# Kernel tuning notes

Hardware: AMD Instinct MI355X
Metric: run time of the kernel (lower is better)

The kernel has to match this reference:

```python
import jax, jax.numpy as jnp
import numpy as np
from jax import lax

B, T, J = 32, 256, 24

def _build_adj(n):
    parent = [-1,0,0,0,1,2,3,4,5,6,7,8,9,9,9,12,13,14,16,17,18,19,20,21]
    a = np.eye(n, dtype=np.float32)
    for c in range(min(n, len(parent))):
        p = parent[c]
        if 0 <= p < n:
            a[c, p] = 1.0
            a[p, c] = 1.0
    if n > len(parent):
        for j in range(len(parent), n - 1):
            a[j, j + 1] = 1.0
            a[j + 1, j] = 1.0
    d = np.clip(a.sum(1, keepdims=True), 1.0, None)
    return jnp.asarray(a / d)

ADJ = _build_adj(J)  # [J, J] degree-normalized SMPL adjacency


def _axis_angle_to_rot6d(aa):
    # aa: [..., 3] -> [..., 6] (first two columns of rotation matrix, row-major)
    angle = jnp.linalg.norm(aa, axis=-1)
    axis = aa / (angle[..., None] + 1e-8)
    x, y, z = axis[..., 0], axis[..., 1], axis[..., 2]
    zeros = jnp.zeros_like(x)
    K = jnp.stack([zeros, -z, y, z, zeros, -x, -y, x, zeros], axis=-1)
    K = K.reshape(axis.shape[:-1] + (3, 3))
    eye = jnp.eye(3, dtype=aa.dtype)
    cos = jnp.cos(angle)[..., None, None]
    sin = jnp.sin(angle)[..., None, None]
    outer = axis[..., :, None] * axis[..., None, :]
    rot = cos * eye + (1.0 - cos) * outer + sin * K
    return rot[..., :2].reshape(aa.shape[:-1] + (6,))


def _bn(x, p, eps=1e-5):
    # inference BatchNorm2d; p = stacked [gamma, beta, mean, var], each [C]
    g, b, m, v = p
    s = g / jnp.sqrt(v + eps)
    return x * s[None, :, None, None] + (b - m * s)[None, :, None, None]


def _block(x, gcn_w, gcn_b, bn1, tcn_w, tcn_b, bn2, res_w=None, res_b=None):
    # 1x1 conv (pointwise channel mix)
    y = jnp.einsum('oc,bctj->botj', gcn_w, x) + gcn_b[None, :, None, None]
    # graph aggregation over joints
    y = jnp.einsum('bctj,jk->bctk', y, ADJ)
    y = jax.nn.relu(_bn(y, bn1))
    # temporal conv (3,1), padding (1,0); dropout is identity at inference
    y = lax.conv_general_dilated(y, tcn_w, (1, 1), ((1, 1), (0, 0)),
                                 dimension_numbers=('NCHW', 'OIHW', 'NCHW'))
    y = _bn(y + tcn_b[None, :, None, None], bn2)
    if res_w is None:
        r = x
    else:
        r = jnp.einsum('oc,bctj->botj', res_w, x) + res_b[None, :, None, None]
    return jax.nn.relu(y + r)


def setup_inputs() -> dict:
    key = jax.random.key(0)
    ks = iter(jax.random.split(key, 64))
    def rn(shape, s=0.05):
        return jax.random.normal(next(ks), shape, jnp.float32) * s
    def bnp(c):
        g = jax.random.uniform(next(ks), (c,), jnp.float32) * 0.5 + 0.75
        b = rn((c,), 0.1)
        m = rn((c,), 0.1)
        v = jax.random.uniform(next(ks), (c,), jnp.float32) * 0.5 + 0.5
        return jnp.stack([g, b, m, v])
    return {
        'x': jax.random.normal(next(ks), (B, T, J, 3), jnp.float32),
        'b1_gcn_w': rn((128, 6)), 'b1_gcn_b': rn((128,)), 'b1_bn1': bnp(128),
        'b1_tcn_w': rn((128, 128, 3, 1)), 'b1_tcn_b': rn((128,)), 'b1_bn2': bnp(128),
        'b1_res_w': rn((128, 6)), 'b1_res_b': rn((128,)),
        'b2_gcn_w': rn((128, 128)), 'b2_gcn_b': rn((128,)), 'b2_bn1': bnp(128),
        'b2_tcn_w': rn((128, 128, 3, 1)), 'b2_tcn_b': rn((128,)), 'b2_bn2': bnp(128),
        'b3_gcn_w': rn((256, 128)), 'b3_gcn_b': rn((256,)), 'b3_bn1': bnp(256),
        'b3_tcn_w': rn((256, 256, 3, 1)), 'b3_tcn_b': rn((256,)), 'b3_bn2': bnp(256),
        'b3_res_w': rn((256, 128)), 'b3_res_b': rn((256,)),
        'out_w': rn((512, 256)), 'out_b': rn((512,)),
    }


def reference(x, b1_gcn_w, b1_gcn_b, b1_bn1, b1_tcn_w, b1_tcn_b, b1_bn2, b1_res_w, b1_res_b,
              b2_gcn_w, b2_gcn_b, b2_bn1, b2_tcn_w, b2_tcn_b, b2_bn2,
              b3_gcn_w, b3_gcn_b, b3_bn1, b3_tcn_w, b3_tcn_b, b3_bn2, b3_res_w, b3_res_b,
              out_w, out_b):
    rot6d = _axis_angle_to_rot6d(x)                 # [B,T,J,6]
    f = jnp.transpose(rot6d, (0, 3, 1, 2))          # [B,6,T,J]
    f = _block(f, b1_gcn_w, b1_gcn_b, b1_bn1, b1_tcn_w, b1_tcn_b, b1_bn2, b1_res_w, b1_res_b)
    f = _block(f, b2_gcn_w, b2_gcn_b, b2_bn1, b2_tcn_w, b2_tcn_b, b2_bn2)
    f = _block(f, b3_gcn_w, b3_gcn_b, b3_bn1, b3_tcn_w, b3_tcn_b, b3_bn2, b3_res_w, b3_res_b)
    pooled = f.mean(axis=(2, 3))                    # [B,256]
    mu = pooled @ out_w.T + out_b                   # [B,512]
    return mu
```

## Files before the change

### kernel.cpp

```cpp
#include <hip/hip_runtime.h>
#include <math.h>

#define J_ 24
#define T_ 256
#define B_ 32

typedef short short8v __attribute__((ext_vector_type(8)));
typedef float f32x4  __attribute__((ext_vector_type(4)));

__device__ __forceinline__ short f2bf(float f) {
    unsigned u = __float_as_uint(f);
    u += 0x7fffu + ((u >> 16) & 1u);
    return (short)(u >> 16);
}
__device__ __forceinline__ float bf2f(short s) {
    return __uint_as_float(((unsigned)(unsigned short)s) << 16);
}

__device__ __constant__ int d_parent[24] = {-1,0,0,0,1,2,3,4,5,6,7,8,9,9,9,12,13,14,16,17,18,19,20,21};

__global__ void adj_init_kernel(float* __restrict__ adj_out) {
    __shared__ float s_adj[576];
    const int tid = threadIdx.x;
    for (int i = tid; i < 576; i += 256) {
        const int j = i / 24, k = i % 24;
        float a = (j == k || d_parent[k] == j || d_parent[j] == k) ? 1.f : 0.f;
        float d = 0.f;
        for (int kk = 0; kk < 24; ++kk)
            d += (j == kk || d_parent[kk] == j || d_parent[j] == kk) ? 1.f : 0.f;
        const float v = a / fmaxf(d, 1.f);
        s_adj[i] = v;
        adj_out[i] = v;
    }
    __syncthreads();
    if (tid < 24) {
        float cs = 0.f;
        for (int j = 0; j < 24; ++j) cs += s_adj[j*24 + tid];
        adj_out[576 + tid] = cs;
        int n = 0;
        for (int j = 0; j < 24; ++j) {
            const float w = s_adj[j*24 + tid];
            if (w != 0.f && n < 8) {
                adj_out[600 + tid*8 + n] = w;
                adj_out[792 + tid*8 + n] = (float)j;
                ++n;
            }
        }
        for (; n < 8; ++n) { adj_out[600 + tid*8 + n] = 0.f; adj_out[792 + tid*8 + n] = 0.f; }
    }
}

__global__ __launch_bounds__(256) void prep_kernel(
    const float* __restrict__ w1t, const float* __restrict__ bn1_2,
    const float* __restrict__ w2t, const float* __restrict__ bn2_2,
    const float* __restrict__ w3t, const float* __restrict__ bn3_2,
    const float* __restrict__ g2w, const float* __restrict__ bn2_1,
    const float* __restrict__ g3w, const float* __restrict__ bn3_1,
    const float* __restrict__ r3w,
    short* __restrict__ wt1b, short* __restrict__ wt2b, short* __restrict__ wt3b,
    short* __restrict__ gw2b, short* __restrict__ gw3b, short* __restrict__ rw3b)
{
    const int i = blockIdx.x * 256 + threadIdx.x;
    if (i < 49152) {
        const int o = i / 384, r = i % 384, dt = r / 128, c = r % 128;
        const float s = bn1_2[o] * rsqrtf(bn1_2[384 + o] + 1e-5f);
        wt1b[i] = f2bf(s * w1t[(o*128 + c)*3 + dt]);
    } else if (i < 98304) {
        const int j = i - 49152;
        const int o = j / 384, r = j % 384, dt = r / 128, c = r % 128;
        const float s = bn2_2[o] * rsqrtf(bn2_2[384 + o] + 1e-5f);
        wt2b[j] = f2bf(s * w2t[(o*128 + c)*3 + dt]);
    } else if (i < 294912) {
        const int j = i - 98304;
        const int o = j / 768, r = j % 768, dt = r / 256, c = r % 256;
        const float s = bn3_2[o] * rsqrtf(bn3_2[768 + o] + 1e-5f);
        wt3b[j] = f2bf(s * w3t[(o*256 + c)*3 + dt]);
    } else if (i < 311296) {
        const int j = i - 294912;
        const int o = j / 128;
        const float s = bn2_1[o] * rsqrtf(bn2_1[384 + o] + 1e-5f);
        gw2b[j] = f2bf(s * g2w[j]);
    } else if (i < 344064) {
        const int j = i - 311296;
        const int o = j / 128;
        const float s = bn3_1[o] * rsqrtf(bn3_1[768 + o] + 1e-5f);
        gw3b[j] = f2bf(s * g3w[j]);
    } else if (i < 376832) {
        const int j = i - 344064;
        rw3b[j] = f2bf(r3w[j]);
    }
}

#define LDS_SZ   52320
#define FA_OFF   26112
#define X6_OFF   40320
#define XA6_OFF  44928
#define TBL_OFF  50688

__global__ __launch_bounds__(512) void block1_kernel(
    const float* __restrict__ x,
    const float* __restrict__ gw1, const float* __restrict__ gb1, const float* __restrict__ bn1,
    const float* __restrict__ rw1, const float* __restrict__ rb1,
    const float* __restrict__ bn12, const float* __restrict__ tb1, const short* __restrict__ wt1b,
    const short* __restrict__ gw2b, const float* __restrict__ gb2, const float* __restrict__ bn21,
    const float* __restrict__ adjp,
    short* __restrict__ f1_out, short* __restrict__ h2_out)
{
    __shared__ char smem[LDS_SZ];
    float* s_x6  = (float*)(smem + X6_OFF);
    float* s_xa6 = (float*)(smem + XA6_OFF);
    float* s_cw  = (float*)(smem + TBL_OFF);
    int*   s_ci  = (int*)  (smem + TBL_OFF + 768);
    float* s_cs  = (float*)(smem + TBL_OFF + 1536);

    const int r0 = blockIdx.x * 96;
    const int bstart = (r0 / 6144) * 6144;
    const int bend = bstart + 6144;
    const int tid = threadIdx.x;
    const int l = tid & 63, wid = tid >> 6;
    const int m0w = (wid >> 2) * 48;
    const int n0w = (wid & 3) * 32;
    const int lr = l & 15, lk = l >> 4;

    if (tid < 192) { s_cw[tid] = adjp[600 + tid]; s_ci[tid] = (int)adjp[792 + tid]; }
    else if (tid < 216) s_cs[tid - 192] = adjp[576 + (tid - 192)];
    if (tid < 144) {
        const int gr = r0 - 24 + tid;
        float o0=0,o1=0,o2=0,o3=0,o4=0,o5=0;
        if (gr >= bstart && gr < bend) {
            const float ax = x[gr*3+0], ay = x[gr*3+1], az = x[gr*3+2];
            const float angle = sqrtf(ax*ax + ay*ay + az*az);
            const float inv = 1.f / (angle + 1e-8f);
            const float ux = ax*inv, uy = ay*inv, uz = az*inv;
            const float c = cosf(angle), s = sinf(angle), omc = 1.f - c;
            o0 = c + omc*ux*ux;   o1 = omc*ux*uy - s*uz;
            o2 = omc*uy*ux + s*uz; o3 = c + omc*uy*uy;
            o4 = omc*uz*ux - s*uy; o5 = omc*uz*uy + s*ux;
        }
        float* p = s_x6 + tid*8;
        p[0]=o0; p[1]=o1; p[2]=o2; p[3]=o3; p[4]=o4; p[5]=o5;
    }
    __syncthreads();
    for (int idx = tid; idx < 864; idx += 512) {
        const int hr = idx / 6, c = idx % 6;
        const int k = hr % 24, sl = (hr / 24) * 24;
        float a = 0.f;
        #pragma unroll
        for (int u = 0; u < 8; ++u)
            a = fmaf(s_cw[k*8+u], s_x6[(sl + s_ci[k*8+u])*8 + c], a);
        s_xa6[hr*8 + c] = a;
    }
    __syncthreads();
    {
        const int og = (tid & 15) * 8;
        const int rg0 = tid >> 4;
        float wgf[48], s1v[8], t1v[8], g1v[8];
        {
            const float4* gwp = (const float4*)(gw1 + og*6);
            #pragma unroll
            for (int i = 0; i < 12; ++i) ((float4*)wgf)[i] = gwp[i];
            #pragma unroll
            for (int e = 0; e < 8; ++e) {
                const int o = og + e;
                const float s1 = bn1[o] * rsqrtf(bn1[384 + o] + 1e-5f);
                s1v[e] = s1;
                t1v[e] = bn1[128 + o] - bn1[256 + o] * s1;
                g1v[e] = s1 * gb1[o];
            }
        }
        for (int hr = rg0; hr < 144; hr += 32) {
            const int gr = r0 - 24 + hr;
            short8v hv = {0,0,0,0,0,0,0,0};
            if (gr >= bstart && gr < bend) {
                const float4 v4 = *(const float4*)(s_xa6 + hr*8);
                const float2 v2 = *(const float2*)(s_xa6 + hr*8 + 4);
                const float cs = s_cs[hr % 24];
                #pragma unroll
                for (int e = 0; e < 8; ++e) {
                    float a = v4.x * wgf[e*6+0];
                    a = fmaf(v4.y, wgf[e*6+1], a);
                    a = fmaf(v4.z, wgf[e*6+2], a);
                    a = fmaf(v4.w, wgf[e*6+3], a);
                    a = fmaf(v2.x, wgf[e*6+4], a);
                    a = fmaf(v2.y, wgf[e*6+5], a);
                    hv[e] = f2bf(fmaxf(s1v[e]*a + t1v[e] + g1v[e]*cs, 0.f));
                }
            }
            *(short8v*)(smem + hr*256 + ((og*2) ^ ((hr&7)<<4))) = hv;
        }
    }
    __syncthreads();
    f32x4 acc[3][2];
    #pragma unroll
    for (int mi = 0; mi < 3; ++mi)
        #pragma unroll
        for (int ni = 0; ni < 2; ++ni) acc[mi][ni] = (f32x4){0.f,0.f,0.f,0.f};
    #pragma unroll
    for (int dt = 0; dt < 3; ++dt) {
        #pragma unroll
        for (int kc = 0; kc < 4; ++kc) {
            short8v bfr[2], afr[3];
            #pragma unroll
            for (int ni = 0; ni < 2; ++ni) {
                const int n = n0w + ni*16 + lr;
                bfr[ni] = *(const short8v*)(wt1b + (size_t)n*384 + dt*128 + kc*32 + lk*8);
            }
            #pragma unroll
            for (int mi = 0; mi < 3; ++mi) {
                const int row = m0w + dt*24 + mi*16 + lr;
                afr[mi] = *(const short8v*)(smem + row*256 + ((kc*64 + lk*16) ^ ((row&7)<<4)));
            }
            #pragma unroll
            for (int mi = 0; mi < 3; ++mi)
                #pragma unroll
                for (int ni = 0; ni < 2; ++ni)
                    acc[mi][ni] = __builtin_amdgcn_mfma_f32_16x16x32_bf16(afr[mi], bfr[ni], acc[mi][ni], 0, 0, 0);
        }
    }
    __syncthreads();
    #pragma unroll
    for (int ni = 0; ni < 2; ++ni) {
        const int o = n0w + ni*16 + lr;
        const float s2 = bn12[o] * rsqrtf(bn12[384 + o] + 1e-5f);
        const float bias = (bn12[128 + o] - bn12[256 + o]*s2) + s2*tb1[o];
        float wr[6];
        #pragma unroll
        for (int c = 0; c < 6; ++c) wr[c] = rw1[o*6 + c];
        const float rb = rb1[o];
        #pragma unroll
        for (int mi = 0; mi < 3; ++mi)
            #pragma unroll
            for (int rg = 0; rg < 4; ++rg) {
                const int rl = m0w + mi*16 + lk*4 + rg;
                const float4 v4 = *(const float4*)(s_x6 + (rl+24)*8);
                const float2 v2 = *(const float2*)(s_x6 + (rl+24)*8 + 4);
                float r = fmaf(v4.x, wr[0], rb);
                r = fmaf(v4.y, wr[1], r);
                r = fmaf(v4.z, wr[2], r);
                r = fmaf(v4.w, wr[3], r);
                r = fmaf(v2.x, wr[4], r);
                r = fmaf(v2.y, wr[5], r);
                const short hv = f2bf(fmaxf(acc[mi][ni][rg] + bias + r, 0.f));
                f1_out[(size_t)(r0 + rl)*128 + o] = hv;
                *(short*)(smem + rl*272 + o*2) = hv;
            }
    }
    __syncthreads();
    for (int task = tid; task < 96*16; task += 512) {
        const int row = task >> 4, cg = task & 15;
        const int k = row % 24, sl = (row / 24) * 24;
        float a[8] = {0,0,0,0,0,0,0,0};
        #pragma unroll
        for (int u = 0; u < 8; ++u) {
            const float wgt = s_cw[k*8+u];
            const short8v v = *(const short8v*)(smem + (sl + s_ci[k*8+u])*272 + cg*16);
            #pragma unroll
            for (int e = 0; e < 8; ++e) a[e] = fmaf(wgt, bf2f(v[e]), a[e]);
        }
        short8v o8;
        #pragma unroll
        for (int e = 0; e < 8; ++e) o8[e] = f2bf(a[e]);
        *(short8v*)(smem + FA_OFF + row*256 + ((cg*16) ^ ((row&7)<<4))) = o8;
    }
    __syncthreads();
    #pragma unroll
    for (int mi = 0; mi < 3; ++mi)
        #pragma unroll
        for (int ni = 0; ni < 2; ++ni) acc[mi][ni] = (f32x4){0.f,0.f,0.f,0.f};
    #pragma unroll
    for (int kc = 0; kc < 4; ++kc) {
        short8v bfr[2], afr[3];
        #pragma unroll
        for (int ni = 0; ni < 2; ++ni) {
            const int n = n0w + ni*16 + lr;
            bfr[ni] = *(const short8v*)(gw2b + (size_t)n*128 + kc*32 + lk*8);
        }
        #pragma unroll
        for (int mi = 0; mi < 3; ++mi) {
            const int row = m0w + mi*16 + lr;
            afr[mi] = *(const short8v*)(smem + FA_OFF + row*256 + ((kc*64 + lk*16) ^ ((row&7)<<4)));
        }
        #pragma unroll
        for (int mi = 0; mi < 3; ++mi)
            #pragma unroll
            for (int ni = 0; ni < 2; ++ni)
                acc[mi][ni] = __builtin_amdgcn_mfma_f32_16x16x32_bf16(afr[mi], bfr[ni], acc[mi][ni], 0, 0, 0);
    }
    #pragma unroll
    for (int ni = 0; ni < 2; ++ni) {
        const int o = n0w + ni*16 + lr;
        const float s = bn21[o] * rsqrtf(bn21[384 + o] + 1e-5f);
        const float t = bn21[128 + o] - bn21[256 + o]*s;
        const float g = s * gb2[o];
        #pragma unroll
        for (int mi = 0; mi < 3; ++mi)
            #pragma unroll
            for (int rg = 0; rg < 4; ++rg) {
                const int rl = m0w + mi*16 + lk*4 + rg;
                h2_out[(size_t)(r0 + rl)*128 + o] = f2bf(fmaxf(acc[mi][ni][rg] + t + g*s_cs[rl % 24], 0.f));
            }
    }
}

__global__ __launch_bounds__(512) void block2_kernel(
    const short* __restrict__ h2, const short* __restrict__ wt2b,
    const float* __restrict__ bn22, const float* __restrict__ tb2,
    const short* __restrict__ f1,
    const short* __restrict__ gw3b, const float* __restrict__ gb3, const float* __restrict__ bn31,
    const float* __restrict__ adjp,
    short* __restrict__ f2_out, short* __restrict__ h3_out)
{
    __shared__ char smem[LDS_SZ];
    float* s_cw  = (float*)(smem + TBL_OFF);
    int*   s_ci  = (int*)  (smem + TBL_OFF + 768);
    float* s_cs  = (float*)(smem + TBL_OFF + 1536);

    const int r0 = blockIdx.x * 96;
    const int bstart = (r0 / 6144) * 6144;
    const int bend = bstart + 6144;
    const int tid = threadIdx.x;
    const int l = tid & 63, wid = tid >> 6;
    const int m0w = (wid >> 2) * 48;
    const int lr = l & 15, lk = l >> 4;

    if (tid < 192) { s_cw[tid] = adjp[600 + tid]; s_ci[tid] = (int)adjp[792 + tid]; }
    else if (tid < 216) s_cs[tid - 192] = adjp[576 + (tid - 192)];
    for (int ch = tid; ch < 144*16; ch += 512) {
        const int row = ch >> 4, cg = ch & 15;
        const int gr = r0 - 24 + row;
        float4 v = make_float4(0.f,0.f,0.f,0.f);
        if (gr >= bstart && gr < bend)
            v = *(const float4*)(h2 + (size_t)gr*128 + cg*8);
        *(float4*)(smem + row*256 + ((cg*16) ^ ((row&7)<<4))) = v;
    }
    __syncthreads();
    {
        const int n0w = (wid & 3) * 32;
        f32x4 acc[3][2];
        #pragma unroll
        for (int mi = 0; mi < 3; ++mi)
            #pragma unroll
            for (int ni = 0; ni < 2; ++ni) acc[mi][ni] = (f32x4){0.f,0.f,0.f,0.f};
        #pragma unroll
        for (int dt = 0; dt < 3; ++dt) {
            #pragma unroll
            for (int kc = 0; kc < 4; ++kc) {
                short8v bfr[2], afr[3];
                #pragma unroll
                for (int ni = 0; ni < 2; ++ni) {
                    const int n = n0w + ni*16 + lr;
                    bfr[ni] = *(const short8v*)(wt2b + (size_t)n*384 + dt*128 + kc*32 + lk*8);
                }
                #pragma unroll
                for (int mi = 0; mi < 3; ++mi) {
                    const int row = m0w + dt*24 + mi*16 + lr;
                    afr[mi] = *(const short8v*)(smem + row*256 + ((kc*64 + lk*16) ^ ((row&7)<<4)));
                }
                #pragma unroll
                for (int mi = 0; mi < 3; ++mi)
                    #pragma unroll
                    for (int ni = 0; ni < 2; ++ni)
                        acc[mi][ni] = __builtin_amdgcn_mfma_f32_16x16x32_bf16(afr[mi], bfr[ni], acc[mi][ni], 0, 0, 0);
            }
        }
        __syncthreads();
        #pragma unroll
        for (int ni = 0; ni < 2; ++ni) {
            const int o = n0w + ni*16 + lr;
            const float s = bn22[o] * rsqrtf(bn22[384 + o] + 1e-5f);
            const float bias = (bn22[128 + o] - bn22[256 + o]*s) + s*tb2[o];
            #pragma unroll
            for (int mi = 0; mi < 3; ++mi)
                #pragma unroll
                for (int rg = 0; rg < 4; ++rg) {
                    const int rl = m0w + mi*16 + lk*4 + rg;
                    const float res = bf2f(f1[(size_t)(r0 + rl)*128 + o]);
                    const short hv = f2bf(fmaxf(acc[mi][ni][rg] + bias + res, 0.f));
                    *(short*)(smem + rl*272 + o*2) = hv;
                    f2_out[(size_t)(r0 + rl)*128 + o] = hv;
                }
        }
    }
    __syncthreads();
    for (int task = tid; task < 96*16; task += 512) {
        const int row = task >> 4, cg = task & 15;
        const int k = row % 24, sl = (row / 24) * 24;
        float a[8] = {0,0,0,0,0,0,0,0};
        #pragma unroll
        for (int u = 0; u < 8; ++u) {
            const float wgt = s_cw[k*8+u];
            const short8v v = *(const short8v*)(smem + (sl + s_ci[k*8+u])*272 + cg*16);
            #pragma unroll
            for (int e = 0; e < 8; ++e) a[e] = fmaf(wgt, bf2f(v[e]), a[e]);
        }
        short8v o8;
        #pragma unroll
        for (int e = 0; e < 8; ++e) o8[e] = f2bf(a[e]);
        *(short8v*)(smem + FA_OFF + row*256 + ((cg*16) ^ ((row&7)<<4))) = o8;
    }
    __syncthreads();
    {
        const int n0w = (wid & 3) * 64;
        f32x4 acc[3][4];
        #pragma unroll
        for (int mi = 0; mi < 3; ++mi)
            #pragma unroll
            for (int ni = 0; ni < 4; ++ni) acc[mi][ni] = (f32x4){0.f,0.f,0.f,0.f};
        #pragma unroll
        for (int kc = 0; kc < 4; ++kc) {
            short8v bfr[4], afr[3];
            #pragma unroll
            for (int ni = 0; ni < 4; ++ni) {
                const int n = n0w + ni*16 + lr;
                bfr[ni] = *(const short8v*)(gw3b + (size_t)n*128 + kc*32 + lk*8);
            }
            #pragma unroll
            for (int mi = 0; mi < 3; ++mi) {
                const int row = m0w + mi*16 + lr;
                afr[mi] = *(const short8v*)(smem + FA_OFF + row*256 + ((kc*64 + lk*16) ^ ((row&7)<<4)));
            }
            #pragma unroll
            for (int mi = 0; mi < 3; ++mi)
                #pragma unroll
                for (int ni = 0; ni < 4; ++ni)
                    acc[mi][ni] = __builtin_amdgcn_mfma_f32_16x16x32_bf16(afr[mi], bfr[ni], acc[mi][ni], 0, 0, 0);
        }
        #pragma unroll
        for (int ni = 0; ni < 4; ++ni) {
            const int o = n0w + ni*16 + lr;
            const float s = bn31[o] * rsqrtf(bn31[768 + o] + 1e-5f);
            const float t = bn31[256 + o] - bn31[512 + o]*s;
            const float g = s * gb3[o];
            #pragma unroll
            for (int mi = 0; mi < 3; ++mi)
                #pragma unroll
                for (int rg = 0; rg < 4; ++rg) {
                    const int rl = m0w + mi*16 + lk*4 + rg;
                    h3_out[(size_t)(r0 + rl)*256 + o] = f2bf(fmaxf(acc[mi][ni][rg] + t + g*s_cs[rl % 24], 0.f));
                }
        }
    }
}

__global__ __launch_bounds__(512) void conv3_pool_kernel(
    const short* __restrict__ A, const short* __restrict__ Bw,
    const float* __restrict__ bn, const float* __restrict__ tb,
    const short* __restrict__ f2, const short* __restrict__ rw3b, const float* __restrict__ rb3,
    float* __restrict__ pooled)
{
    __shared__ char lds[240 * 256];
    const int cpx = gridDim.x >> 3;
    const int bid = blockIdx.x;
    const int tile = (bid % 8) * cpx + bid / 8;
    const int r0 = tile * 192;
    const int bb = r0 / 6144;
    const int bstart = bb * 6144, bend = bstart + 6144;
    const int tid = threadIdx.x, l = tid & 63, wid = tid >> 6;
    const int m0w = (wid >> 2) * 96;
    const int n0w = (wid & 3) * 64;
    const int lr = l & 15, lk = l >> 4;

    f32x4 acc[6][4];
    #pragma unroll
    for (int mi = 0; mi < 6; ++mi)
        #pragma unroll
        for (int ni = 0; ni < 4; ++ni) acc[mi][ni] = (f32x4){0.f,0.f,0.f,0.f};

    for (int p = 0; p < 2; ++p) {
        if (p) __syncthreads();
        for (int ch = tid; ch < 240 * 16; ch += 512) {
            const int row = ch >> 4, c16 = ch & 15;
            const int gr = r0 - 24 + row;
            float4 v = make_float4(0.f,0.f,0.f,0.f);
            if (gr >= bstart && gr < bend)
                v = *(const float4*)(A + (size_t)gr * 256 + p * 128 + c16 * 8);
            *(float4*)(lds + row * 256 + ((c16 * 16) ^ ((row & 7) << 4))) = v;
        }
        __syncthreads();
        #pragma unroll
        for (int dt = 0; dt < 3; ++dt) {
            #pragma unroll
            for (int kc = 0; kc < 4; ++kc) {
                short8v bfr[4], afr[6];
                #pragma unroll
                for (int ni = 0; ni < 4; ++ni) {
                    const int n = n0w + ni * 16 + lr;
                    bfr[ni] = *(const short8v*)(Bw + (size_t)n * 768 + dt * 256 + p * 128 + kc * 32 + lk * 8);
                }
                #pragma unroll
                for (int mi = 0; mi < 6; ++mi) {
                    const int row = m0w + dt * 24 + mi * 16 + lr;
                    afr[mi] = *(const short8v*)(lds + row * 256 + ((kc * 64 + lk * 16) ^ ((row & 7) << 4)));
                }
                #pragma unroll
                for (int mi = 0; mi < 6; ++mi)
                    #pragma unroll
                    for (int ni = 0; ni < 4; ++ni)
                        acc[mi][ni] = __builtin_amdgcn_mfma_f32_16x16x32_bf16(afr[mi], bfr[ni], acc[mi][ni], 0, 0, 0);
            }
        }
    }
    __syncthreads();
    for (int ch = tid; ch < 192 * 16; ch += 512) {
        const int row = ch >> 4, c16 = ch & 15;
        const float4 v = *(const float4*)(f2 + (size_t)(r0 + row) * 128 + c16 * 8);
        *(float4*)(lds + row * 256 + ((c16 * 16) ^ ((row & 7) << 4))) = v;
    }
    __syncthreads();
    #pragma unroll
    for (int kc = 0; kc < 4; ++kc) {
        short8v bfr[4], afr[6];
        #pragma unroll
        for (int ni = 0; ni < 4; ++ni) {
            const int n = n0w + ni * 16 + lr;
            bfr[ni] = *(const short8v*)(rw3b + (size_t)n * 128 + kc * 32 + lk * 8);
        }
        #pragma unroll
        for (int mi = 0; mi < 6; ++mi) {
            const int row = m0w + mi * 16 + lr;
            afr[mi] = *(const short8v*)(lds + row * 256 + ((kc * 64 + lk * 16) ^ ((row & 7) << 4)));
        }
        #pragma unroll
        for (int mi = 0; mi < 6; ++mi)
            #pragma unroll
            for (int ni = 0; ni < 4; ++ni)
                acc[mi][ni] = __builtin_amdgcn_mfma_f32_16x16x32_bf16(afr[mi], bfr[ni], acc[mi][ni], 0, 0, 0);
    }

    float psum[4] = {0.f, 0.f, 0.f, 0.f};
    #pragma unroll
    for (int ni = 0; ni < 4; ++ni) {
        const int o = n0w + ni * 16 + lr;
        const float s = bn[o] * rsqrtf(bn[768 + o] + 1e-5f);
        const float t = bn[256 + o] - bn[512 + o] * s;
        const float bias = s * tb[o] + t + rb3[o];
        #pragma unroll
        for (int mi = 0; mi < 6; ++mi)
            #pragma unroll
            for (int rg = 0; rg < 4; ++rg)
                psum[ni] += fmaxf(acc[mi][ni][rg] + bias, 0.f);
    }
    #pragma unroll
    for (int ni = 0; ni < 4; ++ni) {
        float v = psum[ni];
        v += __shfl_xor(v, 16);
        v += __shfl_xor(v, 32);
        if (l < 16) atomicAdd(pooled + (size_t)bb * 256 + (n0w + ni * 16 + l), v);
    }
}

__global__ __launch_bounds__(256) void head_kernel(const float* __restrict__ pooled_sums,
    const float* __restrict__ ow, const float* __restrict__ ob, float* __restrict__ outp) {
    __shared__ float pooled[256];
    const int b = blockIdx.x, tid = threadIdx.x;
    pooled[tid] = pooled_sums[(size_t)b*256 + tid] * (1.f/6144.f);
    __syncthreads();
    for (int rep = 0; rep < 2; ++rep) {
        const int oo = rep*256 + tid;
        float a = ob[oo];
        const float4* wr = (const float4*)(ow + (size_t)oo*256);
        for (int c4 = 0; c4 < 64; ++c4) {
            const float4 w = wr[c4];
            const float4 p = *(const float4*)&pooled[c4*4];
            a += w.x*p.x + w.y*p.y + w.z*p.z + w.w*p.w;
        }
        outp[(size_t)b*512 + oo] = a;
    }
}

extern "C" void kernel_launch(void* const* d_in, const int* in_sizes, int n_in,
                              void* d_out, int out_size, void* d_ws, size_t ws_size,
                              hipStream_t stream)
{
    const float* x        = (const float*)d_in[0];
    const float* b1_gcn_w = (const float*)d_in[1];
    const float* b1_gcn_b = (const float*)d_in[2];
    const float* b1_bn1   = (const float*)d_in[3];
    const float* b1_tcn_w = (const float*)d_in[4];
    const float* b1_tcn_b = (const float*)d_in[5];
    const float* b1_bn2   = (const float*)d_in[6];
    const float* b1_res_w = (const float*)d_in[7];
    const float* b1_res_b = (const float*)d_in[8];
    const float* b2_gcn_w = (const float*)d_in[9];
    const float* b2_gcn_b = (const float*)d_in[10];
    const float* b2_bn1   = (const float*)d_in[11];
    const float* b2_tcn_w = (const float*)d_in[12];
    const float* b2_tcn_b = (const float*)d_in[13];
    const float* b2_bn2   = (const float*)d_in[14];
    const float* b3_gcn_w = (const float*)d_in[15];
    const float* b3_gcn_b = (const float*)d_in[16];
    const float* b3_bn1   = (const float*)d_in[17];
    const float* b3_tcn_w = (const float*)d_in[18];
    const float* b3_tcn_b = (const float*)d_in[19];
    const float* b3_bn2   = (const float*)d_in[20];
    const float* b3_res_w = (const float*)d_in[21];
    const float* b3_res_b = (const float*)d_in[22];
    const float* out_w    = (const float*)d_in[23];
    const float* out_b    = (const float*)d_in[24];

    char* w = (char*)d_ws;
    float* adjp = (float*)w;   w += 4096;
    short* wt1b = (short*)w;   w += 98304;
    short* wt2b = (short*)w;   w += 98304;
    short* wt3b = (short*)w;   w += 393216;
    short* gw2b = (short*)w;   w += 32768;
    short* gw3b = (short*)w;   w += 65536;
    short* rw3b = (short*)w;   w += 65536;
    float* pooled = (float*)w; w += 32768;
    const size_t fixed = (size_t)(w - (char*)d_ws);

    int G = 1;
    {
        const int tiers[6] = {32, 16, 8, 4, 2, 1};
        for (int ti = 0; ti < 6; ++ti) {
            const size_t need = fixed + (size_t)tiers[ti] * 6291456ull;
            if (need <= ws_size) { G = tiers[ti]; break; }
        }
    }
    const size_t MG = (size_t)G * 6144;

    short* f1 = (short*)w;
    short* h2 = f1 + MG*128;
    short* h3 = h2 + MG*128;
    short* f2 = f1;

    hipMemsetAsync(pooled, 0, 32*256*sizeof(float), stream);
    adj_init_kernel<<<1, 256, 0, stream>>>(adjp);
    prep_kernel<<<1472, 256, 0, stream>>>(b1_tcn_w, b1_bn2, b2_tcn_w, b2_bn2, b3_tcn_w, b3_bn2,
                                          b2_gcn_w, b2_bn1, b3_gcn_w, b3_bn1, b3_res_w,
                                          wt1b, wt2b, wt3b, gw2b, gw3b, rw3b);

    for (int b0 = 0; b0 < B_; b0 += G) {
        block1_kernel<<<64*G, 512, 0, stream>>>(
            x + (size_t)b0*6144*3,
            b1_gcn_w, b1_gcn_b, b1_bn1, b1_res_w, b1_res_b,
            b1_bn2, b1_tcn_b, wt1b,
            gw2b, b2_gcn_b, b2_bn1, adjp, f1, h2);
        block2_kernel<<<64*G, 512, 0, stream>>>(
            h2, wt2b, b2_bn2, b2_tcn_b, f1,
            gw3b, b3_gcn_b, b3_bn1, adjp, f2, h3);
        conv3_pool_kernel<<<32*G, 512, 0, stream>>>(
            h3, wt3b, b3_bn2, b3_tcn_b, f2, rw3b, b3_res_b, pooled + (size_t)b0*256);
    }

    head_kernel<<<B_, 256, 0, stream>>>(pooled, out_w, out_b, (float*)d_out);
}
```

Measured before the change: 454.4 us.

## Replace sparse joint-graph aggregation with MFMA block-diagonal adjacency matmul

Builds a 96x96 block-diagonal bf16 adjacency matrix (four time steps of 24 joints) once at init. In block1 and block2 the scalar 8-neighbour gather-FMA aggregation is replaced by an MFMA matmul of this matrix against a channel-major transposed tile in LDS. The intermediate tile layout changes to channel-major with a 208-byte stride, and LDS offsets are adjusted. This moves the aggregation onto matrix cores but does about 4x redundant work on zero blocks and adds a global read of the adjacency matrix plus an extra barrier.

```diff
diff --git a/kernel.cpp b/kernel.cpp
--- a/kernel.cpp
+++ b/kernel.cpp
@@ -19,7 +19,7 @@
 
 __device__ __constant__ int d_parent[24] = {-1,0,0,0,1,2,3,4,5,6,7,8,9,9,9,12,13,14,16,17,18,19,20,21};
 
-__global__ void adj_init_kernel(float* __restrict__ adj_out) {
+__global__ void adj_init_kernel(float* __restrict__ adj_out, short* __restrict__ amix) {
     __shared__ float s_adj[576];
     const int tid = threadIdx.x;
     for (int i = tid; i < 576; i += 256) {
@@ -47,6 +47,13 @@
             }
         }
         for (; n < 8; ++n) { adj_out[600 + tid*8 + n] = 0.f; adj_out[792 + tid*8 + n] = 0.f; }
+    }
+    __syncthreads();
+    for (int i = tid; i < 96*96; i += 256) {
+        const int r = i / 96, j = i % 96;
+        float v = 0.f;
+        if (r / 24 == j / 24) v = s_adj[(j % 24) * 24 + (r % 24)];
+        amix[i] = f2bf(v);
     }
 }
 
@@ -91,11 +98,12 @@
     }
 }
 
-#define LDS_SZ   52320
-#define FA_OFF   26112
+#define LDS_SZ   52832
+#define FA_OFF   26624
+#define FT_STRIDE 208
 #define X6_OFF   40320
 #define XA6_OFF  44928
-#define TBL_OFF  50688
+#define TBL_OFF  51200
 
 __global__ __launch_bounds__(512) void block1_kernel(
     const float* __restrict__ x,
@@ -103,7 +111,7 @@
     const float* __restrict__ rw1, const float* __restrict__ rb1,
     const float* __restrict__ bn12, const float* __restrict__ tb1, const short* __restrict__ wt1b,
     const short* __restrict__ gw2b, const float* __restrict__ gb2, const float* __restrict__ bn21,
-    const float* __restrict__ adjp,
+    const float* __restrict__ adjp, const short* __restrict__ amix,
     short* __restrict__ f1_out, short* __restrict__ h2_out)
 {
     __shared__ char smem[LDS_SZ];
@@ -242,25 +250,48 @@
                 r = fmaf(v2.y, wr[5], r);
                 const short hv = f2bf(fmaxf(acc[mi][ni][rg] + bias + r, 0.f));
                 f1_out[(size_t)(r0 + rl)*128 + o] = hv;
-                *(short*)(smem + rl*272 + o*2) = hv;
-            }
-    }
-    __syncthreads();
-    for (int task = tid; task < 96*16; task += 512) {
-        const int row = task >> 4, cg = task & 15;
-        const int k = row % 24, sl = (row / 24) * 24;
-        float a[8] = {0,0,0,0,0,0,0,0};
-        #pragma unroll
-        for (int u = 0; u < 8; ++u) {
-            const float wgt = s_cw[k*8+u];
-            const short8v v = *(const short8v*)(smem + (sl + s_ci[k*8+u])*272 + cg*16);
-            #pragma unroll
-            for (int e = 0; e < 8; ++e) a[e] = fmaf(wgt, bf2f(v[e]), a[e]);
-        }
-        short8v o8;
-        #pragma unroll
-        for (int e = 0; e < 8; ++e) o8[e] = f2bf(a[e]);
-        *(short8v*)(smem + FA_OFF + row*256 + ((cg*16) ^ ((row&7)<<4))) = o8;
+                *(short*)(smem + o*FT_STRIDE + rl*2) = hv;
+            }
+    }
+    __syncthreads();
+    {
+        f32x4 pacc[3][2];
+        #pragma unroll
+        for (int mi = 0; mi < 3; ++mi)
+            #pragma unroll
+            for (int ni = 0; ni < 2; ++ni) pacc[mi][ni] = (f32x4){0.f,0.f,0.f,0.f};
+        #pragma unroll
+        for (int kc = 0; kc < 3; ++kc) {
+            short8v bfr[2], afr[3];
+            #pragma unroll
+            for (int ni = 0; ni < 2; ++ni) {
+                const int ch = n0w + ni*16 + lr;
+                bfr[ni] = *(const short8v*)(smem + ch*FT_STRIDE + kc*64 + lk*16);
+            }
+            #pragma unroll
+            for (int mi = 0; mi < 3; ++mi) {
+                const int row = m0w + mi*16 + lr;
+                afr[mi] = *(const short8v*)(amix + row*96 + kc*32 + lk*8);
+            }
+            #pragma unroll
+            for (int mi = 0; mi < 3; ++mi)
+                #pragma unroll
+                for (int ni = 0; ni < 2; ++ni)
+                    pacc[mi][ni] = __builtin_amdgcn_mfma_f32_16x16x32_bf16(afr[mi], bfr[ni], pacc[mi][ni], 0, 0, 0);
+        }
+        __syncthreads();
+        #pragma unroll
+        for (int ni = 0; ni < 2; ++ni) {
+            const int ch2 = (n0w + ni*16 + lr) * 2;
+            #pragma unroll
+            for (int mi = 0; mi < 3; ++mi)
+                #pragma unroll
+                for (int rg = 0; rg < 4; ++rg) {
+                    const int row = m0w + mi*16 + lk*4 + rg;
+                    *(short*)(smem + FA_OFF + row*256 + ((ch2 & 0xF0) ^ ((row&7)<<4)) + (ch2 & 14)) =
+                        f2bf(pacc[mi][ni][rg]);
+                }
+        }
     }
     __syncthreads();
     #pragma unroll
@@ -307,12 +338,10 @@
     const float* __restrict__ bn22, const float* __restrict__ tb2,
     const short* __restrict__ f1,
     const short* __restrict__ gw3b, const float* __restrict__ gb3, const float* __restrict__ bn31,
-    const float* __restrict__ adjp,
+    const float* __restrict__ adjp, const short* __restrict__ amix,
     short* __restrict__ f2_out, short* __restrict__ h3_out)
 {
     __shared__ char smem[LDS_SZ];
-    float* s_cw  = (float*)(smem + TBL_OFF);
-    int*   s_ci  = (int*)  (smem + TBL_OFF + 768);
     float* s_cs  = (float*)(smem + TBL_OFF + 1536);
 
     const int r0 = blockIdx.x * 96;
@@ -323,8 +352,7 @@
     const int m0w = (wid >> 2) * 48;
     const int lr = l & 15, lk = l >> 4;
 
-    if (tid < 192) { s_cw[tid] = adjp[600 + tid]; s_ci[tid] = (int)adjp[792 + tid]; }
-    else if (tid < 216) s_cs[tid - 192] = adjp[576 + (tid - 192)];
+    if (tid < 24) s_cs[tid] = adjp[576 + tid];
     for (int ch = tid; ch < 144*16; ch += 512) {
         const int row = ch >> 4, cg = ch & 15;
         const int gr = r0 - 24 + row;
@@ -376,27 +404,51 @@
                     const int rl = m0w + mi*16 + lk*4 + rg;
                     const float res = bf2f(f1[(size_t)(r0 + rl)*128 + o]);
                     const short hv = f2bf(fmaxf(acc[mi][ni][rg] + bias + res, 0.f));
-                    *(short*)(smem + rl*272 + o*2) = hv;
+                    *(short*)(smem + o*FT_STRIDE + rl*2) = hv;
                     f2_out[(size_t)(r0 + rl)*128 + o] = hv;
                 }
         }
     }
     __syncthreads();
-    for (int task = tid; task < 96*16; task += 512) {
-        const int row = task >> 4, cg = task & 15;
-        const int k = row % 24, sl = (row / 24) * 24;
-        float a[8] = {0,0,0,0,0,0,0,0};
-        #pragma unroll
-        for (int u = 0; u < 8; ++u) {
-            const float wgt = s_cw[k*8+u];
-            const short8v v = *(const short8v*)(smem + (sl + s_ci[k*8+u])*272 + cg*16);
-            #pragma unroll
-            for (int e = 0; e < 8; ++e) a[e] = fmaf(wgt, bf2f(v[e]), a[e]);
-        }
-        short8v o8;
-        #pragma unroll
-        for (int e = 0; e < 8; ++e) o8[e] = f2bf(a[e]);
-        *(short8v*)(smem + FA_OFF + row*256 + ((cg*16) ^ ((row&7)<<4))) = o8;
+    {
+        const int n0w = (wid & 3) * 32;
+        f32x4 pacc[3][2];
+        #pragma unroll
+        for (int mi = 0; mi < 3; ++mi)
+            #pragma unroll
+            for (int ni = 0; ni < 2; ++ni) pacc[mi][ni] = (f32x4){0.f,0.f,0.f,0.f};
+        #pragma unroll
+        for (int kc = 0; kc < 3; ++kc) {
+            short8v bfr[2], afr[3];
+            #pragma unroll
+            for (int ni = 0; ni < 2; ++ni) {
+                const int ch = n0w + ni*16 + lr;
+                bfr[ni] = *(const short8v*)(smem + ch*FT_STRIDE + kc*64 + lk*16);
+            }
+            #pragma unroll
+            for (int mi = 0; mi < 3; ++mi) {
+                const int row = m0w + mi*16 + lr;
+                afr[mi] = *(const short8v*)(amix + row*96 + kc*32 + lk*8);
+            }
+            #pragma unroll
+            for (int mi = 0; mi < 3; ++mi)
+                #pragma unroll
+                for (int ni = 0; ni < 2; ++ni)
+                    pacc[mi][ni] = __builtin_amdgcn_mfma_f32_16x16x32_bf16(afr[mi], bfr[ni], pacc[mi][ni], 0, 0, 0);
+        }
+        __syncthreads();
+        #pragma unroll
+        for (int ni = 0; ni < 2; ++ni) {
+            const int ch2 = (n0w + ni*16 + lr) * 2;
+            #pragma unroll
+            for (int mi = 0; mi < 3; ++mi)
+                #pragma unroll
+                for (int rg = 0; rg < 4; ++rg) {
+                    const int row = m0w + mi*16 + lk*4 + rg;
+                    *(short*)(smem + FA_OFF + row*256 + ((ch2 & 0xF0) ^ ((row&7)<<4)) + (ch2 & 14)) =
+                        f2bf(pacc[mi][ni][rg]);
+                }
+        }
     }
     __syncthreads();
     {
@@ -606,6 +658,7 @@
     short* gw2b = (short*)w;   w += 32768;
     short* gw3b = (short*)w;   w += 65536;
     short* rw3b = (short*)w;   w += 65536;
+    short* amixb = (short*)w;  w += 18432;
     float* pooled = (float*)w; w += 32768;
     const size_t fixed = (size_t)(w - (char*)d_ws);
 
@@ -625,7 +678,7 @@
     short* f2 = f1;
 
     hipMemsetAsync(pooled, 0, 32*256*sizeof(float), stream);
-    adj_init_kernel<<<1, 256, 0, stream>>>(adjp);
+    adj_init_kernel<<<1, 256, 0, stream>>>(adjp, amixb);
     prep_kernel<<<1472, 256, 0, stream>>>(b1_tcn_w, b1_bn2, b2_tcn_w, b2_bn2, b3_tcn_w, b3_bn2,
                                           b2_gcn_w, b2_bn1, b3_gcn_w, b3_bn1, b3_res_w,
                                           wt1b, wt2b, wt3b, gw2b, gw3b, rw3b);
@@ -635,10 +688,10 @@
             x + (size_t)b0*6144*3,
             b1_gcn_w, b1_gcn_b, b1_bn1, b1_res_w, b1_res_b,
             b1_bn2, b1_tcn_b, wt1b,
-            gw2b, b2_gcn_b, b2_bn1, adjp, f1, h2);
+            gw2b, b2_gcn_b, b2_bn1, adjp, amixb, f1, h2);
         block2_kernel<<<64*G, 512, 0, stream>>>(
             h2, wt2b, b2_bn2, b2_tcn_b, f1,
-            gw3b, b3_gcn_b, b3_bn1, adjp, f2, h3);
+            gw3b, b3_gcn_b, b3_bn1, adjp, amixb, f2, h3);
         conv3_pool_kernel<<<32*G, 512, 0, stream>>>(
             h3, wt3b, b3_bn2, b3_tcn_b, f2, rw3b, b3_res_b, pooled + (size_t)b0*256);
     }
```

After: 432.0 us. 1.05x faster.
